# Kernel optimization log

Hardware: AMD Instinct MI355X
Metric: run time of the kernel (lower is better)

The kernel has to match this reference:

```python
import jax, jax.numpy as jnp
import numpy as np

B, T, N = 2, 256, 512
H, S, C = 64, 8, 8
DYN = 4


def setup_inputs() -> dict:
    key = jax.random.key(0)
    ks = jax.random.split(key, 12)
    sc = 0.05
    return {
        "x": jax.random.normal(ks[0], (B, T, N), jnp.float32),
        "mask": (jax.random.uniform(ks[1], (B, T, N)) < 0.2).astype(jnp.float32),
        "static_context": jax.random.normal(ks[2], (N, S), jnp.float32),
        "node_coords": jax.random.normal(ks[3], (N, C), jnp.float32),
        "W1": jax.random.normal(ks[4], (DYN + S, H), jnp.float32) * sc,
        "b1": jnp.zeros((H,), jnp.float32),
        "W2": jax.random.normal(ks[5], (H, H), jnp.float32) * sc,
        "b2": jnp.zeros((H,), jnp.float32),
        "We1": jax.random.normal(ks[6], (4 * H, H), jnp.float32) * sc,
        "be1": jnp.zeros((H,), jnp.float32),
        "We2": jax.random.normal(ks[7], (H, 1), jnp.float32) * sc,
        "be2": jnp.zeros((1,), jnp.float32),
        "self_loop_logit": jnp.float32(0.5),
        "prior_strength": jnp.float32(1.0),
        "similarity_strength": jnp.float32(1.0),
        "temperature": jnp.float32(0.7),
    }


def reference(x, mask, static_context, node_coords, W1, b1, W2, b2,
              We1, be1, We2, be2, self_loop_logit, prior_strength,
              similarity_strength, temperature):
    Bv, Tv, Nv = x.shape
    # ---- dynamic per-node context over time ----
    observed = 1.0 - mask                                   # [B,T,N]
    count = jnp.maximum(observed.sum(axis=1), 1.0)          # [B,N]
    mean = (x * observed).sum(axis=1) / count               # [B,N]
    centered = (x - mean[:, None, :]) * observed
    std = jnp.sqrt((centered ** 2).sum(axis=1) / count + 1e-6)
    t_idx = jnp.arange(Tv, dtype=x.dtype)[None, :, None]
    latest = jnp.argmax(t_idx * observed, axis=1)           # [B,N] int
    last = jnp.take_along_axis(x, latest[:, None, :], axis=1)[:, 0, :]
    missing_ratio = mask.mean(axis=1)
    dyn = jnp.stack([mean, std, last, missing_ratio], axis=-1)  # [B,N,4]
    # ---- node encoder ----
    static = jnp.broadcast_to(static_context[None], (Bv, Nv, static_context.shape[-1]))
    feats = jnp.concatenate([dyn, static], axis=-1)
    h = jax.nn.relu(feats @ W1 + b1)
    h = jax.nn.relu(h @ W2 + b2)                            # [B,N,H]
    hn = h / jnp.maximum(jnp.linalg.norm(h, axis=-1, keepdims=True), 1e-12)
    # ---- edge MLP on pair features [h_i, h_j, |h_i-h_j|, h_i*h_j] ----
    # split first-layer weight into the four blocks so h_i/h_j terms are O(N)
    Wi, Wj, Wa, Wp = jnp.split(We1, 4, axis=0)              # each [H,H]
    pre_i = h @ Wi                                          # [B,N,H]
    pre_j = h @ Wj
    hi = h[:, :, None, :]                                   # [B,N,1,H]
    hj = h[:, None, :, :]                                   # [B,1,N,H]
    hidden = jax.nn.relu(pre_i[:, :, None, :] + pre_j[:, None, :, :]
                         + jnp.abs(hi - hj) @ Wa + (hi * hj) @ Wp + be1)
    edge_logits = (hidden @ We2 + be2)[..., 0]              # [B,N,N]
    # ---- cosine similarity + distance prior ----
    cos = jnp.einsum('bnh,bmh->bnm', hn, hn)
    eye = jnp.eye(Nv, dtype=x.dtype)
    off = 1.0 - eye
    diff = node_coords[:, None, :] - node_coords[None, :, :]
    dist = jnp.sqrt(jnp.maximum((diff ** 2).sum(-1), 1e-12))
    prior = (1.0 / (1.0 + dist)) * off                      # [N,N]
    # ---- combine, softmax, symmetrize, row-normalize ----
    logits = (edge_logits * off
              + jax.nn.softplus(prior_strength) * prior[None]
              + jax.nn.softplus(similarity_strength) * (cos * off))
    logits = logits + eye[None] * jax.nn.softplus(self_loop_logit)
    temp = jax.nn.softplus(temperature) + 1e-4
    adj = jax.nn.softmax(logits / temp, axis=-1)
    adj = 0.5 * (adj + jnp.swapaxes(adj, -1, -2))
    adj = adj / jnp.maximum(adj.sum(axis=-1, keepdims=True), 1e-6)
    return adj
```

## Files before the change

kernel.cpp:

```cpp
#include <hip/hip_runtime.h>
#include <hip/hip_bf16.h>
#include <math.h>

#define NB 2
#define NT 256
#define NN 512
#define NH 64
#define NS 8
#define NC 8

#define OFF_H      0
#define OFF_PVEC   65536
#define OFF_HF16   131072
#define OFF_HNF16  163840
#define OFF_WA16   196608
#define OFF_WJF    198656
#define OFF_WPF    202752
#define OFF_GEXT   206848
#define OFF_UNSYM  731136

typedef __attribute__((ext_vector_type(8))) _Float16 h8;
typedef __attribute__((ext_vector_type(2))) __fp16 fp16x2;
typedef __attribute__((ext_vector_type(4))) float f32x4;
typedef __attribute__((ext_vector_type(4))) unsigned u4;
typedef __attribute__((ext_vector_type(2))) unsigned u2;

__device__ __forceinline__ float softplusf(float x){
  if (x > 20.f) return x;
  return log1pf(expf(x));
}

__device__ __forceinline__ unsigned pkh(float a, float b){
  fp16x2 h = __builtin_amdgcn_cvt_pkrtz(a, b);
  return __builtin_bit_cast(unsigned, h);
}

template<int CTRL>
__device__ __forceinline__ float dpp_addf(float x){
  int xi = __builtin_bit_cast(int, x);
  int yi = __builtin_amdgcn_update_dpp(0, xi, CTRL, 0xF, 0xF, true);
  return x + __builtin_bit_cast(float, yi);
}
__device__ __forceinline__ float row16_sum(float x){
  x = dpp_addf<0xB1>(x);
  x = dpp_addf<0x4E>(x);
  x = dpp_addf<0x141>(x);
  x = dpp_addf<0x140>(x);
  return x;
}

__global__ __launch_bounds__(256) void k_front(
    const float* __restrict__ x, const float* __restrict__ mask,
    const float* __restrict__ sctx,
    const float* __restrict__ W1, const float* __restrict__ b1,
    const float* __restrict__ W2, const float* __restrict__ b2,
    const float* __restrict__ We1, const float* __restrict__ be1,
    float* __restrict__ hg, float* __restrict__ pvec,
    unsigned* __restrict__ hf16, unsigned* __restrict__ hn16,
    short* __restrict__ wa16, float* __restrict__ wjf,
    float* __restrict__ wpf){
  int blk = blockIdx.x;
  int tid = threadIdx.x;

  if (blk >= 256){
    int pidx = (blk - 256)*256 + tid;
    int e    = pidx & 7;
    int lane = (pidx >> 3) & 63;
    int frag = (pidx >> 9) & 7;
    int nt = frag & 3, ks = frag >> 2;
    int kg = lane >> 4, q = lane & 15;
    int kk = ks*32 + kg*8 + e;
    int c  = nt*16 + q;
    if (pidx < 4096){
      _Float16 v = (_Float16)We1[(128 + kk)*NH + c];
      wa16[pidx] = __builtin_bit_cast(short, v);
    } else if (pidx < 8192){
      wjf[pidx - 4096] = We1[(64 + kk)*NH + c];
    } else {
      wpf[pidx - 8192] = We1[(192 + kk)*NH + c];
    }
    return;
  }

  int b  = blk >> 7;
  int n0 = (blk & 127) * 4;

  int nl = tid & 3;
  int ts = tid >> 2;
  int n  = n0 + nl;

  float cnt = 0.f, sx = 0.f, sxx = 0.f;
  int lastt = 0;
  for (int t = ts*4; t < ts*4 + 4; ++t){
    int idx = (b*NT + t)*NN + n;
    float xv = x[idx];
    float mv = mask[idx];
    bool obs = (mv < 0.5f);
    if (obs){ cnt += 1.f; sx += xv; sxx += xv*xv; lastt = t; }
  }
  #pragma unroll
  for (int m = 4; m < 64; m <<= 1){
    cnt   += __shfl_xor(cnt,  m);
    sx    += __shfl_xor(sx,   m);
    sxx   += __shfl_xor(sxx,  m);
    lastt  = max(lastt, __shfl_xor(lastt, m));
  }
  int w = tid >> 6;
  __shared__ float r_cnt[4][4], r_sx[4][4], r_sxx[4][4];
  __shared__ int   r_lt[4][4];
  __shared__ float s_dyn[4][4];
  if ((tid & 63) < 4){
    r_cnt[w][nl] = cnt; r_sx[w][nl] = sx; r_sxx[w][nl] = sxx; r_lt[w][nl] = lastt;
  }
  __syncthreads();
  if (tid < 4){
    float c = 0.f, s1 = 0.f, s2 = 0.f; int lt = 0;
    #pragma unroll
    for (int ww = 0; ww < 4; ++ww){
      c  += r_cnt[ww][tid]; s1 += r_sx[ww][tid]; s2 += r_sxx[ww][tid];
      lt  = max(lt, r_lt[ww][tid]);
    }
    float cc   = fmaxf(c, 1.f);
    float mean = s1 / cc;
    float var  = s2 / cc - mean*mean;
    float stdv = sqrtf(fmaxf(var, 0.f) + 1e-6f);
    float last = x[(b*NT + lt)*NN + n0 + tid];
    float mr   = 1.f - c * (1.f/(float)NT);
    s_dyn[tid][0] = mean; s_dyn[tid][1] = stdv; s_dyn[tid][2] = last; s_dyn[tid][3] = mr;
  }
  __syncthreads();

  int c = tid & 63;
  int gn = n0 + w;
  int bn = b*NN + gn;
  __shared__ float s_f[4][12];
  __shared__ float s_h1[4][64];
  __shared__ float s_h2[4][64];

  if (c < 4)       s_f[w][c] = s_dyn[w][c];
  else if (c < 12) s_f[w][c] = sctx[gn*NS + (c-4)];
  __syncthreads();

  float a = b1[c];
  #pragma unroll
  for (int k = 0; k < 12; ++k) a = fmaf(s_f[w][k], W1[k*NH + c], a);
  s_h1[w][c] = fmaxf(a, 0.f);
  __syncthreads();

  float a2 = b2[c];
  #pragma unroll 8
  for (int k = 0; k < 64; ++k) a2 = fmaf(s_h1[w][k], W2[k*NH + c], a2);
  a2 = fmaxf(a2, 0.f);

  float sq = a2*a2;
  #pragma unroll
  for (int m = 1; m < 64; m <<= 1) sq += __shfl_xor(sq, m);
  float inv = 1.f / fmaxf(sqrtf(sq), 1e-12f);

  s_h2[w][c] = a2;
  __syncthreads();

  float pi = be1[c];
  #pragma unroll 8
  for (int k = 0; k < 64; ++k) pi = fmaf(s_h2[w][k], We1[k*NH + c], pi);

  hg  [bn*64 + c] = a2;
  pvec[bn*64 + c] = pi;
  if (c < 32){
    float e0 = s_h2[w][2*c], e1 = s_h2[w][2*c + 1];
    hf16[bn*32 + c] = pkh(e0, e1);
    hn16[bn*32 + c] = pkh(e0*inv, e1*inv);
  }
}

__global__ __launch_bounds__(256) void k_extra(
    const unsigned* __restrict__ hn16, const float* __restrict__ coords,
    const float* __restrict__ s_ss, const float* __restrict__ s_ps,
    const float* __restrict__ be2, float* __restrict__ gext){
  int b   = blockIdx.x;
  int i0  = blockIdx.y * 16;
  int jq  = blockIdx.z;
  int tid = threadIdx.x;
  int w   = tid >> 6;
  int lane = tid & 63;
  float spss = softplusf(s_ss[0]);
  float spps = softplusf(s_ps[0]);
  float be2v = be2[0];

  const u4* hv = (const u4*)hn16;
  int arow = i0 + (lane & 15);
  u4 a0 = hv[(b*NN + arow)*8 + (lane >> 4)];
  u4 a1 = hv[(b*NN + arow)*8 + (lane >> 4) + 4];
  h8 A0 = __builtin_bit_cast(h8, a0);
  h8 A1 = __builtin_bit_cast(h8, a1);

  #pragma unroll
  for (int t = 0; t < 2; ++t){
    int j0 = (jq*8 + w*2 + t) * 16;
    int jrow = j0 + (lane & 15);
    u4 b0 = hv[(b*NN + jrow)*8 + (lane >> 4)];
    u4 b1 = hv[(b*NN + jrow)*8 + (lane >> 4) + 4];
    f32x4 acc = (f32x4){0.f, 0.f, 0.f, 0.f};
    acc = __builtin_amdgcn_mfma_f32_16x16x32_f16(A0, __builtin_bit_cast(h8, b0), acc, 0, 0, 0);
    acc = __builtin_amdgcn_mfma_f32_16x16x32_f16(A1, __builtin_bit_cast(h8, b1), acc, 0, 0, 0);

    int jc = j0 + (lane & 15);
    float4 cj0 = *(const float4*)(coords + jc*NC);
    float4 cj1 = *(const float4*)(coords + jc*NC + 4);
    #pragma unroll
    for (int r = 0; r < 4; ++r){
      int irow = i0 + (lane >> 4)*4 + r;
      float4 ci0 = *(const float4*)(coords + irow*NC);
      float4 ci1 = *(const float4*)(coords + irow*NC + 4);
      float dd = 0.f;
      dd = fmaf(ci0.x-cj0.x, ci0.x-cj0.x, dd);
      dd = fmaf(ci0.y-cj0.y, ci0.y-cj0.y, dd);
      dd = fmaf(ci0.z-cj0.z, ci0.z-cj0.z, dd);
      dd = fmaf(ci0.w-cj0.w, ci0.w-cj0.w, dd);
      dd = fmaf(ci1.x-cj1.x, ci1.x-cj1.x, dd);
      dd = fmaf(ci1.y-cj1.y, ci1.y-cj1.y, dd);
      dd = fmaf(ci1.z-cj1.z, ci1.z-cj1.z, dd);
      dd = fmaf(ci1.w-cj1.w, ci1.w-cj1.w, dd);
      float dist  = sqrtf(fmaxf(dd, 1e-12f));
      float prior = (irow == jc) ? 0.f : spps / (1.f + dist);
      gext[(size_t)(b*NN + irow)*NN + jc] = fmaf(spss, acc[r], be2v + prior);
    }
  }
}

__global__ __launch_bounds__(512, 4) void k_logits(
    const float* __restrict__ hg, const float* __restrict__ pvec,
    const unsigned* __restrict__ hf16, const short* __restrict__ wa16,
    const float* __restrict__ wjf, const float* __restrict__ wpf,
    const float* __restrict__ We2, const float* __restrict__ gext,
    const float* __restrict__ s_sl, const float* __restrict__ s_tp,
    float* __restrict__ unsym){
  int blk = blockIdx.x;
  int b  = blk >> 8;
  int ip = (blk & 255) * 2;
  int tid  = threadIdx.x;
  int w    = tid >> 6;
  int lane = tid & 63;
  int q    = lane & 15;
  int kg   = lane >> 4;

  __shared__ __align__(16) float s_hi[2][64];
  __shared__ __align__(16) float lrow[2][NN];
  __shared__ __align__(16) unsigned lds_wa[2048];
  __shared__ __align__(16) unsigned lds_cw[2][2048];
  __shared__ __align__(16) unsigned s_hj[8][16*34 + 2];
  __shared__ float red[32];

  float spsl = softplusf(s_sl[0]);
  float invt = 1.f / (softplusf(s_tp[0]) + 1e-4f);

  if (tid < 128)
    s_hi[tid >> 6][tid & 63] = hg[(b*NN + ip + (tid >> 6))*64 + (tid & 63)];
  __syncthreads();

  {
    int frag = tid >> 6;
    int l2   = tid & 63;
    const u4* wsrc = (const u4*)wa16;
    *(u4*)&lds_wa[(frag*64 + l2)*4] = wsrc[frag*64 + l2];

    int ch0 = (frag >> 2)*32 + (l2 >> 4)*8;
    const float* wj = wjf + (frag*64 + l2)*8;
    const float* wp = wpf + (frag*64 + l2)*8;
    #pragma unroll
    for (int r = 0; r < 2; ++r){
      u4 u;
      #pragma unroll
      for (int d = 0; d < 4; ++d){
        float v0 = fmaf(s_hi[r][ch0 + 2*d],     wp[2*d],     wj[2*d]);
        float v1 = fmaf(s_hi[r][ch0 + 2*d + 1], wp[2*d + 1], wj[2*d + 1]);
        u[d] = pkh(v0, v1);
      }
      *(u4*)&lds_cw[r][(frag*64 + l2)*4] = u;
    }
  }

  const u4* hfv = (const u4*)hf16;
  u4 hiA[2][2];
  #pragma unroll
  for (int r = 0; r < 2; ++r){
    hiA[r][0] = hfv[(b*NN + ip + r)*8 + kg];
    hiA[r][1] = hfv[(b*NN + ip + r)*8 + kg + 4];
  }

  float pv4[2][4], we2q[4];
  #pragma unroll
  for (int nt = 0; nt < 4; ++nt){
    #pragma unroll
    for (int r = 0; r < 2; ++r)
      pv4[r][nt] = pvec[(b*NN + ip + r)*64 + nt*16 + q];
    we2q[nt] = We2[nt*16 + q];
  }
  __syncthreads();

  unsigned* slice = &s_hj[w][0];
  const u4 absm = (u4){0x7fff7fffu, 0x7fff7fffu, 0x7fff7fffu, 0x7fff7fffu};

  #pragma unroll
  for (int s = 0; s < 4; ++s){
    int it = w + s*8;
    int jbase = it * 16;

    {
      int r8 = lane >> 3, c8 = lane & 7;
      u4 g0 = *(const u4*)((const unsigned*)hf16 + (size_t)(b*NN + jbase + r8)*32 + c8*4);
      u4 g1 = *(const u4*)((const unsigned*)hf16 + (size_t)(b*NN + jbase + 8 + r8)*32 + c8*4);
      unsigned* p0 = slice + r8*34 + c8*4;
      unsigned* p1 = slice + (8 + r8)*34 + c8*4;
      u2 t;
      t.x = g0.x; t.y = g0.y; *(u2*)p0 = t;
      t.x = g0.z; t.y = g0.w; *(u2*)(p0 + 2) = t;
      t.x = g1.x; t.y = g1.y; *(u2*)p1 = t;
      t.x = g1.z; t.y = g1.w; *(u2*)(p1 + 2) = t;
    }

    u4 hj0, hj1;
    {
      unsigned* rp = slice + q*34 + kg*4;
      u2 a0 = *(u2*)rp;
      u2 a1 = *(u2*)(rp + 2);
      u2 b0 = *(u2*)(rp + 16);
      u2 b1 = *(u2*)(rp + 18);
      hj0.x = a0.x; hj0.y = a0.y; hj0.z = a1.x; hj0.w = a1.y;
      hj1.x = b0.x; hj1.y = b0.y; hj1.z = b1.x; hj1.w = b1.y;
    }
    h8 hjv0 = __builtin_bit_cast(h8, hj0);
    h8 hjv1 = __builtin_bit_cast(h8, hj1);

    f32x4 acc[2][4];
    #pragma unroll
    for (int r = 0; r < 2; ++r)
      #pragma unroll
      for (int nt = 0; nt < 4; ++nt)
        acc[r][nt] = (f32x4){pv4[r][nt], pv4[r][nt], pv4[r][nt], pv4[r][nt]};

    #pragma unroll
    for (int nt = 0; nt < 4; ++nt){
      h8 wA0 = __builtin_bit_cast(h8, *(const u4*)&lds_wa[((0*4 + nt)*64 + lane)*4]);
      h8 wA1 = __builtin_bit_cast(h8, *(const u4*)&lds_wa[((1*4 + nt)*64 + lane)*4]);
      #pragma unroll
      for (int r = 0; r < 2; ++r){
        h8 dh0 = __builtin_bit_cast(h8, hiA[r][0]) - hjv0;
        h8 dh1 = __builtin_bit_cast(h8, hiA[r][1]) - hjv1;
        h8 af0 = __builtin_bit_cast(h8, __builtin_bit_cast(u4, dh0) & absm);
        h8 af1 = __builtin_bit_cast(h8, __builtin_bit_cast(u4, dh1) & absm);
        h8 wC0 = __builtin_bit_cast(h8, *(const u4*)&lds_cw[r][((0*4 + nt)*64 + lane)*4]);
        h8 wC1 = __builtin_bit_cast(h8, *(const u4*)&lds_cw[r][((1*4 + nt)*64 + lane)*4]);
        acc[r][nt] = __builtin_amdgcn_mfma_f32_16x16x32_f16(af0, wA0, acc[r][nt], 0, 0, 0);
        acc[r][nt] = __builtin_amdgcn_mfma_f32_16x16x32_f16(af1, wA1, acc[r][nt], 0, 0, 0);
        acc[r][nt] = __builtin_amdgcn_mfma_f32_16x16x32_f16(hjv0, wC0, acc[r][nt], 0, 0, 0);
        acc[r][nt] = __builtin_amdgcn_mfma_f32_16x16x32_f16(hjv1, wC1, acc[r][nt], 0, 0, 0);
      }
    }

    #pragma unroll
    for (int r = 0; r < 2; ++r){
      float part[4] = {0.f, 0.f, 0.f, 0.f};
      #pragma unroll
      for (int nt = 0; nt < 4; ++nt)
        #pragma unroll
        for (int rr = 0; rr < 4; ++rr)
          part[rr] = fmaf(fmaxf(acc[r][nt][rr], 0.f), we2q[nt], part[rr]);
      #pragma unroll
      for (int rr = 0; rr < 4; ++rr) part[rr] = row16_sum(part[rr]);

      if (q < 4){
        int j2 = jbase + kg*4 + q;
        float ps2 = part[0];
        ps2 = (q == 1) ? part[1] : ps2;
        ps2 = (q == 2) ? part[2] : ps2;
        ps2 = (q == 3) ? part[3] : ps2;
        lrow[r][j2] = ps2;
      }
    }
  }
  __syncthreads();

  float ga = gext[(size_t)(b*NN + ip)*NN + tid];
  float gb = gext[(size_t)(b*NN + ip + 1)*NN + tid];
  float va = (tid == ip)     ? spsl : lrow[0][tid] + ga;
  float vb = (tid == ip + 1) ? spsl : lrow[1][tid] + gb;

  float ma = va, mb = vb;
  #pragma unroll
  for (int msk = 1; msk < 64; msk <<= 1){
    ma = fmaxf(ma, __shfl_xor(ma, msk));
    mb = fmaxf(mb, __shfl_xor(mb, msk));
  }
  if (lane == 0){ red[w] = ma; red[8 + w] = mb; }
  __syncthreads();
  ma = red[0]; mb = red[8];
  #pragma unroll
  for (int ww = 1; ww < 8; ++ww){
    ma = fmaxf(ma, red[ww]);
    mb = fmaxf(mb, red[8 + ww]);
  }

  float ea = expf((va - ma) * invt);
  float eb = expf((vb - mb) * invt);
  float sa = ea, sb = eb;
  #pragma unroll
  for (int msk = 1; msk < 64; msk <<= 1){
    sa += __shfl_xor(sa, msk);
    sb += __shfl_xor(sb, msk);
  }
  if (lane == 0){ red[16 + w] = sa; red[24 + w] = sb; }
  __syncthreads();
  sa = red[16]; sb = red[24];
  #pragma unroll
  for (int ww = 1; ww < 8; ++ww){
    sa += red[16 + ww];
    sb += red[24 + ww];
  }

  unsym[(size_t)(b*NN + ip)*NN + tid]       = ea / sa;
  unsym[(size_t)(b*NN + ip + 1)*NN + tid]   = eb / sb;
}

__global__ __launch_bounds__(256) void k_sym(
    const float* __restrict__ u, float* __restrict__ out){
  int blk = blockIdx.x;
  int b = blk >> 9, i = blk & (NN-1);
  int tid = threadIdx.x;
  const float* urow = u + (size_t)(b*NN + i) * NN;
  float v0, v1, rs;
  {
    int j0 = tid, j1 = tid + 256;
    float a1 = urow[j0];
    float a2 = u[(size_t)(b*NN + j0) * NN + i];
    v0 = 0.5f*(a1 + a2);
    float a3 = urow[j1];
    float a4 = u[(size_t)(b*NN + j1) * NN + i];
    v1 = 0.5f*(a3 + a4);
    rs = v0 + v1;
  }
  int lane = tid & 63, w = tid >> 6;
  #pragma unroll
  for (int msk = 1; msk < 64; msk <<= 1) rs += __shfl_xor(rs, msk);
  __shared__ float red[4];
  if (lane == 0) red[w] = rs;
  __syncthreads();
  rs = red[0] + red[1] + red[2] + red[3];
  float inv = 1.f / fmaxf(rs, 1e-6f);
  float* orow = out + (size_t)(b*NN + i) * NN;
  orow[tid]       = v0 * inv;
  orow[tid + 256] = v1 * inv;
}

extern "C" void kernel_launch(void* const* d_in, const int* in_sizes, int n_in,
                              void* d_out, int out_size, void* d_ws, size_t ws_size,
                              hipStream_t stream){
  const float* x      = (const float*)d_in[0];
  const float* mask   = (const float*)d_in[1];
  const float* sctx   = (const float*)d_in[2];
  const float* coords = (const float*)d_in[3];
  const float* W1     = (const float*)d_in[4];
  const float* b1     = (const float*)d_in[5];
  const float* W2     = (const float*)d_in[6];
  const float* b2     = (const float*)d_in[7];
  const float* We1    = (const float*)d_in[8];
  const float* be1    = (const float*)d_in[9];
  const float* We2    = (const float*)d_in[10];
  const float* be2    = (const float*)d_in[11];
  const float* sl     = (const float*)d_in[12];
  const float* ps     = (const float*)d_in[13];
  const float* ss     = (const float*)d_in[14];
  const float* tp     = (const float*)d_in[15];

  float*    ws    = (float*)d_ws;
  float*    hgp   = ws + OFF_H;
  float*    pvecp = ws + OFF_PVEC;
  unsigned* hf16p = (unsigned*)(ws + OFF_HF16);
  unsigned* hn16p = (unsigned*)(ws + OFF_HNF16);
  short*    wa16p = (short*)(ws + OFF_WA16);
  float*    wjfp  = ws + OFF_WJF;
  float*    wpfp  = ws + OFF_WPF;
  float*    gext  = ws + OFF_GEXT;
  float*    unsym = ws + OFF_UNSYM;
  float*    out   = (float*)d_out;

  k_front <<<304, 256, 0, stream>>>(x, mask, sctx, W1, b1, W2, b2, We1, be1,
                                    hgp, pvecp, hf16p, hn16p, wa16p, wjfp, wpfp);
  k_extra <<<dim3(NB, 32, 4), 256, 0, stream>>>(hn16p, coords, ss, ps, be2, gext);
  k_logits<<<NB*NN/2, 512, 0, stream>>>(hgp, pvecp, hf16p, wa16p, wjfp, wpfp,
                                        We2, gext, sl, tp, unsym);
  k_sym   <<<NB*NN, 256, 0, stream>>>(unsym, out);
}
```

Measured before the change: 43.76 us.

## Fuse cosine-similarity and distance-prior kernel into edge-logits kernel

Removes the separate k_extra kernel, which wrote a full B×N×N gext buffer that k_logits then read back. k_logits now computes the distance prior per row pair into shared memory and the cosine term with fdot2 dot products on the already-loaded fp16 h rows, scaled by per-node inverse norms from k_front. This drops one launch and the global round trip of a 2 MB intermediate. In exchange k_logits does extra VALU dot products and cross-lane shuffles, and uses more shared memory.

```diff
diff --git a/kernel.cpp b/kernel.cpp
--- a/kernel.cpp
+++ b/kernel.cpp
@@ -12,12 +12,11 @@
 #define OFF_H      0
 #define OFF_PVEC   65536
 #define OFF_HF16   131072
-#define OFF_HNF16  163840
-#define OFF_WA16   196608
-#define OFF_WJF    198656
-#define OFF_WPF    202752
-#define OFF_GEXT   206848
-#define OFF_UNSYM  731136
+#define OFF_INVN   163840
+#define OFF_WA16   164864
+#define OFF_WJF    166912
+#define OFF_WPF    171008
+#define OFF_UNSYM  175104
 
 typedef __attribute__((ext_vector_type(8))) _Float16 h8;
 typedef __attribute__((ext_vector_type(2))) __fp16 fp16x2;
@@ -33,6 +32,22 @@
 __device__ __forceinline__ unsigned pkh(float a, float b){
   fp16x2 h = __builtin_amdgcn_cvt_pkrtz(a, b);
   return __builtin_bit_cast(unsigned, h);
+}
+
+__device__ __forceinline__ float fdot2u(unsigned a, unsigned b, float c){
+#if __has_builtin(__builtin_amdgcn_fdot2)
+  return __builtin_amdgcn_fdot2(__builtin_bit_cast(fp16x2, a),
+                                __builtin_bit_cast(fp16x2, b), c, false);
+#else
+  fp16x2 av = __builtin_bit_cast(fp16x2, a);
+  fp16x2 bv = __builtin_bit_cast(fp16x2, b);
+  return fmaf((float)av.x, (float)bv.x, fmaf((float)av.y, (float)bv.y, c));
+#endif
+}
+__device__ __forceinline__ float dot8(u4 a, u4 b, float acc){
+  #pragma unroll
+  for (int d = 0; d < 4; ++d) acc = fdot2u(a[d], b[d], acc);
+  return acc;
 }
 
 template<int CTRL>
@@ -56,7 +71,7 @@
     const float* __restrict__ W2, const float* __restrict__ b2,
     const float* __restrict__ We1, const float* __restrict__ be1,
     float* __restrict__ hg, float* __restrict__ pvec,
-    unsigned* __restrict__ hf16, unsigned* __restrict__ hn16,
+    unsigned* __restrict__ hf16, float* __restrict__ invn,
     short* __restrict__ wa16, float* __restrict__ wjf,
     float* __restrict__ wpf){
   int blk = blockIdx.x;
@@ -169,49 +184,54 @@
   if (c < 32){
     float e0 = s_h2[w][2*c], e1 = s_h2[w][2*c + 1];
     hf16[bn*32 + c] = pkh(e0, e1);
-    hn16[bn*32 + c] = pkh(e0*inv, e1*inv);
-  }
-}
-
-__global__ __launch_bounds__(256) void k_extra(
-    const unsigned* __restrict__ hn16, const float* __restrict__ coords,
-    const float* __restrict__ s_ss, const float* __restrict__ s_ps,
-    const float* __restrict__ be2, float* __restrict__ gext){
-  int b   = blockIdx.x;
-  int i0  = blockIdx.y * 16;
-  int jq  = blockIdx.z;
-  int tid = threadIdx.x;
-  int w   = tid >> 6;
+  }
+  if (c == 0) invn[bn] = inv;
+}
+
+__global__ __launch_bounds__(512, 4) void k_logits(
+    const float* __restrict__ hg, const float* __restrict__ pvec,
+    const unsigned* __restrict__ hf16, const float* __restrict__ invn,
+    const short* __restrict__ wa16, const float* __restrict__ wjf,
+    const float* __restrict__ wpf, const float* __restrict__ coords,
+    const float* __restrict__ We2, const float* __restrict__ be2,
+    const float* __restrict__ s_sl, const float* __restrict__ s_ps,
+    const float* __restrict__ s_ss, const float* __restrict__ s_tp,
+    float* __restrict__ unsym){
+  int blk = blockIdx.x;
+  int b  = blk >> 8;
+  int ip = (blk & 255) * 2;
+  int tid  = threadIdx.x;
+  int w    = tid >> 6;
   int lane = tid & 63;
+  int q    = lane & 15;
+  int kg   = lane >> 4;
+
+  __shared__ __align__(16) float s_hi[2][64];
+  __shared__ __align__(16) float s_pri[2][NN];
+  __shared__ __align__(16) float s_invn[NN];
+  __shared__ __align__(16) float lrow[2][NN];
+  __shared__ __align__(16) unsigned lds_wa[2048];
+  __shared__ __align__(16) unsigned lds_cw[2][2048];
+  __shared__ __align__(16) unsigned s_hj[8][16*34 + 2];
+  __shared__ float red[32];
+
+  float spsl = softplusf(s_sl[0]);
+  float spps = softplusf(s_ps[0]);
   float spss = softplusf(s_ss[0]);
-  float spps = softplusf(s_ps[0]);
+  float invt = 1.f / (softplusf(s_tp[0]) + 1e-4f);
   float be2v = be2[0];
 
-  const u4* hv = (const u4*)hn16;
-  int arow = i0 + (lane & 15);
-  u4 a0 = hv[(b*NN + arow)*8 + (lane >> 4)];
-  u4 a1 = hv[(b*NN + arow)*8 + (lane >> 4) + 4];
-  h8 A0 = __builtin_bit_cast(h8, a0);
-  h8 A1 = __builtin_bit_cast(h8, a1);
-
-  #pragma unroll
-  for (int t = 0; t < 2; ++t){
-    int j0 = (jq*8 + w*2 + t) * 16;
-    int jrow = j0 + (lane & 15);
-    u4 b0 = hv[(b*NN + jrow)*8 + (lane >> 4)];
-    u4 b1 = hv[(b*NN + jrow)*8 + (lane >> 4) + 4];
-    f32x4 acc = (f32x4){0.f, 0.f, 0.f, 0.f};
-    acc = __builtin_amdgcn_mfma_f32_16x16x32_f16(A0, __builtin_bit_cast(h8, b0), acc, 0, 0, 0);
-    acc = __builtin_amdgcn_mfma_f32_16x16x32_f16(A1, __builtin_bit_cast(h8, b1), acc, 0, 0, 0);
-
-    int jc = j0 + (lane & 15);
-    float4 cj0 = *(const float4*)(coords + jc*NC);
-    float4 cj1 = *(const float4*)(coords + jc*NC + 4);
-    #pragma unroll
-    for (int r = 0; r < 4; ++r){
-      int irow = i0 + (lane >> 4)*4 + r;
-      float4 ci0 = *(const float4*)(coords + irow*NC);
-      float4 ci1 = *(const float4*)(coords + irow*NC + 4);
+  if (tid < 128)
+    s_hi[tid >> 6][tid & 63] = hg[(b*NN + ip + (tid >> 6))*64 + (tid & 63)];
+  {
+    int j = tid;
+    float4 cj0 = *(const float4*)(coords + j*NC);
+    float4 cj1 = *(const float4*)(coords + j*NC + 4);
+    #pragma unroll
+    for (int r = 0; r < 2; ++r){
+      int i = ip + r;
+      float4 ci0 = *(const float4*)(coords + i*NC);
+      float4 ci1 = *(const float4*)(coords + i*NC + 4);
       float dd = 0.f;
       dd = fmaf(ci0.x-cj0.x, ci0.x-cj0.x, dd);
       dd = fmaf(ci0.y-cj0.y, ci0.y-cj0.y, dd);
@@ -221,41 +241,11 @@
       dd = fmaf(ci1.y-cj1.y, ci1.y-cj1.y, dd);
       dd = fmaf(ci1.z-cj1.z, ci1.z-cj1.z, dd);
       dd = fmaf(ci1.w-cj1.w, ci1.w-cj1.w, dd);
-      float dist  = sqrtf(fmaxf(dd, 1e-12f));
-      float prior = (irow == jc) ? 0.f : spps / (1.f + dist);
-      gext[(size_t)(b*NN + irow)*NN + jc] = fmaf(spss, acc[r], be2v + prior);
-    }
-  }
-}
-
-__global__ __launch_bounds__(512, 4) void k_logits(
-    const float* __restrict__ hg, const float* __restrict__ pvec,
-    const unsigned* __restrict__ hf16, const short* __restrict__ wa16,
-    const float* __restrict__ wjf, const float* __restrict__ wpf,
-    const float* __restrict__ We2, const float* __restrict__ gext,
-    const float* __restrict__ s_sl, const float* __restrict__ s_tp,
-    float* __restrict__ unsym){
-  int blk = blockIdx.x;
-  int b  = blk >> 8;
-  int ip = (blk & 255) * 2;
-  int tid  = threadIdx.x;
-  int w    = tid >> 6;
-  int lane = tid & 63;
-  int q    = lane & 15;
-  int kg   = lane >> 4;
-
-  __shared__ __align__(16) float s_hi[2][64];
-  __shared__ __align__(16) float lrow[2][NN];
-  __shared__ __align__(16) unsigned lds_wa[2048];
-  __shared__ __align__(16) unsigned lds_cw[2][2048];
-  __shared__ __align__(16) unsigned s_hj[8][16*34 + 2];
-  __shared__ float red[32];
-
-  float spsl = softplusf(s_sl[0]);
-  float invt = 1.f / (softplusf(s_tp[0]) + 1e-4f);
-
-  if (tid < 128)
-    s_hi[tid >> 6][tid & 63] = hg[(b*NN + ip + (tid >> 6))*64 + (tid & 63)];
+      float dist = sqrtf(fmaxf(dd, 1e-12f));
+      s_pri[r][j] = (j == i) ? be2v : fmaf(spps, 1.f/(1.f + dist), be2v);
+    }
+    s_invn[j] = invn[b*NN + j];
+  }
   __syncthreads();
 
   {
@@ -296,6 +286,10 @@
       pv4[r][nt] = pvec[(b*NN + ip + r)*64 + nt*16 + q];
     we2q[nt] = We2[nt*16 + q];
   }
+  float invni[2];
+  invni[0] = invn[b*NN + ip];
+  invni[1] = invn[b*NN + ip + 1];
+  int srcl = (lane & 48) | (((lane >> 4) & 3) << 2) | (lane & 3);
   __syncthreads();
 
   unsigned* slice = &s_hj[w][0];
@@ -331,6 +325,13 @@
     }
     h8 hjv0 = __builtin_bit_cast(h8, hj0);
     h8 hjv1 = __builtin_bit_cast(h8, hj1);
+
+    float dotp[2];
+    #pragma unroll
+    for (int r = 0; r < 2; ++r){
+      float d0 = dot8(hiA[r][0], hj0, 0.f);
+      dotp[r]  = dot8(hiA[r][1], hj1, d0);
+    }
 
     f32x4 acc[2][4];
     #pragma unroll
@@ -369,22 +370,26 @@
       #pragma unroll
       for (int rr = 0; rr < 4; ++rr) part[rr] = row16_sum(part[rr]);
 
+      float dp = dotp[r];
+      dp += __shfl_xor(dp, 16);
+      dp += __shfl_xor(dp, 32);
+      float dj = __shfl(dp, srcl);
+
       if (q < 4){
         int j2 = jbase + kg*4 + q;
         float ps2 = part[0];
         ps2 = (q == 1) ? part[1] : ps2;
         ps2 = (q == 2) ? part[2] : ps2;
         ps2 = (q == 3) ? part[3] : ps2;
-        lrow[r][j2] = ps2;
+        float cosv = dj * invni[r] * s_invn[j2];
+        lrow[r][j2] = ps2 + s_pri[r][j2] + spss * cosv;
       }
     }
   }
   __syncthreads();
 
-  float ga = gext[(size_t)(b*NN + ip)*NN + tid];
-  float gb = gext[(size_t)(b*NN + ip + 1)*NN + tid];
-  float va = (tid == ip)     ? spsl : lrow[0][tid] + ga;
-  float vb = (tid == ip + 1) ? spsl : lrow[1][tid] + gb;
+  float va = (tid == ip)     ? spsl : lrow[0][tid];
+  float vb = (tid == ip + 1) ? spsl : lrow[1][tid];
 
   float ma = va, mb = vb;
   #pragma unroll
@@ -476,18 +481,17 @@
   float*    hgp   = ws + OFF_H;
   float*    pvecp = ws + OFF_PVEC;
   unsigned* hf16p = (unsigned*)(ws + OFF_HF16);
-  unsigned* hn16p = (unsigned*)(ws + OFF_HNF16);
+  float*    invnp = ws + OFF_INVN;
   short*    wa16p = (short*)(ws + OFF_WA16);
   float*    wjfp  = ws + OFF_WJF;
   float*    wpfp  = ws + OFF_WPF;
-  float*    gext  = ws + OFF_GEXT;
   float*    unsym = ws + OFF_UNSYM;
   float*    out   = (float*)d_out;
 
   k_front <<<304, 256, 0, stream>>>(x, mask, sctx, W1, b1, W2, b2, We1, be1,
-                                    hgp, pvecp, hf16p, hn16p, wa16p, wjfp, wpfp);
-  k_extra <<<dim3(NB, 32, 4), 256, 0, stream>>>(hn16p, coords, ss, ps, be2, gext);
-  k_logits<<<NB*NN/2, 512, 0, stream>>>(hgp, pvecp, hf16p, wa16p, wjfp, wpfp,
-                                        We2, gext, sl, tp, unsym);
+                                    hgp, pvecp, hf16p, invnp, wa16p, wjfp, wpfp);
+  k_logits<<<NB*NN/2, 512, 0, stream>>>(hgp, pvecp, hf16p, invnp, wa16p, wjfp,
+                                        wpfp, coords, We2, be2, sl, ps, ss, tp,
+                                        unsym);
   k_sym   <<<NB*NN, 256, 0, stream>>>(unsym, out);
 }
```

Measured after the change: 43.47 us. About the same (-0.7%).
